# Performance work log

Hardware: AMD Instinct MI355X
Metric: run time of the kernel (lower is better)

Reference implementation:

```python
import jax, jax.numpy as jnp
import numpy as np

D_IN = 768
D_OUT = 768
NUM_HEADS = 12
HEAD_DIM = D_OUT // NUM_HEADS


def setup_inputs() -> dict:
    key = jax.random.key(0)
    ks = jax.random.split(key, 6)
    s = 1.0 / np.sqrt(D_IN)
    X = jax.random.normal(ks[0], (4, 2048, D_IN), dtype=jnp.float32)
    Wq = jax.random.uniform(ks[1], (D_IN, D_OUT), jnp.float32, -s, s)
    Wk = jax.random.uniform(ks[2], (D_IN, D_OUT), jnp.float32, -s, s)
    Wv = jax.random.uniform(ks[3], (D_IN, D_OUT), jnp.float32, -s, s)
    Wo = jax.random.uniform(ks[4], (D_OUT, D_OUT), jnp.float32, -s, s)
    bo = jax.random.uniform(ks[5], (D_OUT,), jnp.float32, -s, s)
    return {"X": X, "Wq": Wq, "Wk": Wk, "Wv": Wv, "Wo": Wo, "bo": bo}


def reference(X, Wq, Wk, Wv, Wo, bo):
    b, n, _ = X.shape
    # QKV projections, split heads -> [b, h, n, d]
    def split(t):
        return t.reshape(b, n, NUM_HEADS, HEAD_DIM).transpose(0, 2, 1, 3)
    q = split(X @ Wq)
    k = split(X @ Wk)
    v = split(X @ Wv)
    scores = jnp.einsum('bhqd,bhkd->bhqk', q, k) / np.sqrt(HEAD_DIM).astype(np.float32)
    causal = jnp.triu(jnp.ones((n, n), dtype=bool), k=1)
    scores = jnp.where(causal, -jnp.inf, scores)
    attn = jax.nn.softmax(scores, axis=-1)  # dropout p=0 -> identity
    ctx = jnp.einsum('bhqk,bhkd->bhqd', attn, v)
    ctx = ctx.transpose(0, 2, 1, 3).reshape(b, n, D_OUT)
    return ctx @ Wo + bo
```

## Files before the change

### kernel.cpp

```cpp
#include <hip/hip_runtime.h>
#include <stdint.h>

#define B_  4
#define N_  2048
#define D_  768
#define H_  12
#define HD_ 64
#define M_  (B_*N_)

typedef short bf8 __attribute__((ext_vector_type(8)));
typedef float f32x4 __attribute__((ext_vector_type(4)));

static __device__ __forceinline__ unsigned short f2bf(float f) {
    unsigned u = __float_as_uint(f);
    unsigned r = u + 0x7fffu + ((u >> 16) & 1u);
    return (unsigned short)(r >> 16);
}

static __device__ __forceinline__ unsigned pk2bf(float f0, float f1) {
    return ((__float_as_uint(f1) + 0x8000u) & 0xFFFF0000u) |
           ((__float_as_uint(f0) + 0x8000u) >> 16);
}

#if __has_builtin(__builtin_amdgcn_exp2f)
#define EXP2(x) __builtin_amdgcn_exp2f(x)
#else
#define EXP2(x) exp2f(x)
#endif

#define GLOAD_LDS16(gptr, lptr)                                                   \
    __builtin_amdgcn_global_load_lds(                                             \
        (const __attribute__((address_space(1))) void*)(gptr),                    \
        (__attribute__((address_space(3))) void*)(lptr), 16, 0, 0)

#define QSCALE 0.1803368801111204f

__global__ __launch_bounds__(256) void convert_x(const float* __restrict__ X,
                                                 unsigned short* __restrict__ Xb) {
    const size_t i = ((size_t)blockIdx.x * 256 + threadIdx.x) * 8;
    const float4 a = *(const float4*)(X + i);
    const float4 b = *(const float4*)(X + i + 4);
    ushort4 lo, hi;
    lo.x = f2bf(a.x); lo.y = f2bf(a.y); lo.z = f2bf(a.z); lo.w = f2bf(a.w);
    hi.x = f2bf(b.x); hi.y = f2bf(b.y); hi.z = f2bf(b.z); hi.w = f2bf(b.w);
    *(ushort4*)(Xb + i)     = lo;
    *(ushort4*)(Xb + i + 4) = hi;
}

__global__ __launch_bounds__(256) void transpose_w(
    const float* __restrict__ Wq, const float* __restrict__ Wk,
    const float* __restrict__ Wv, const float* __restrict__ Wo,
    unsigned short* __restrict__ Wqt, unsigned short* __restrict__ Wkt,
    unsigned short* __restrict__ Wvt, unsigned short* __restrict__ Wot)
{
    __shared__ float tile[32][33];
    const int z = blockIdx.z;
    const float* W = (z == 0) ? Wq : (z == 1) ? Wk : (z == 2) ? Wv : Wo;
    unsigned short* Wt = (z == 0) ? Wqt : (z == 1) ? Wkt : (z == 2) ? Wvt : Wot;
    const int k0 = blockIdx.x * 32, n0 = blockIdx.y * 32;
    const int tx = threadIdx.x & 31, ty = threadIdx.x >> 5;
    #pragma unroll
    for (int i = 0; i < 4; ++i)
        tile[ty + 8 * i][tx] = W[(size_t)(k0 + ty + 8 * i) * D_ + n0 + tx];
    __syncthreads();
    #pragma unroll
    for (int i = 0; i < 4; ++i)
        Wt[(size_t)(n0 + ty + 8 * i) * D_ + k0 + tx] = f2bf(tile[tx][ty + 8 * i]);
}

__global__ __launch_bounds__(256) void qkv_mfma(
    const unsigned short* __restrict__ Xb,
    const unsigned short* __restrict__ Wqt, const unsigned short* __restrict__ Wkt,
    const unsigned short* __restrict__ Wvt,
    unsigned short* __restrict__ Qb, unsigned short* __restrict__ Kb,
    unsigned short* __restrict__ Vt)
{
    __shared__ unsigned short As[128 * 32];
    __shared__ unsigned short Bs[128 * 32];

    const int t = threadIdx.x;
    const int wave = t >> 6, lane = t & 63;
    const int col = lane & 15, quad = lane >> 4;
    const int wm = (wave & 1) * 64, wn = (wave >> 1) * 64;

    const int m0 = blockIdx.x * 128;
    const int n0 = blockIdx.y * 128;
    const int mat = blockIdx.z;
    const unsigned short* Wt = (mat == 0) ? Wqt : (mat == 1) ? Wkt : Wvt;

    const unsigned short* Ag0 = Xb + (size_t)(m0 + (t >> 2)) * D_ + (t & 3) * 8;
    const unsigned short* Ag1 = Ag0 + (size_t)64 * D_;
    const unsigned short* Bg0 = Wt + (size_t)(n0 + (t >> 2)) * D_ + (t & 3) * 8;
    const unsigned short* Bg1 = Bg0 + (size_t)64 * D_;
    unsigned short* AsW0 = As + wave * 512;
    unsigned short* AsW1 = As + 2048 + wave * 512;
    unsigned short* BsW0 = Bs + wave * 512;
    unsigned short* BsW1 = Bs + 2048 + wave * 512;

    f32x4 acc[4][4] = {};

    for (int k0 = 0; k0 < D_; k0 += 32) {
        __syncthreads();
        GLOAD_LDS16(Ag0 + k0, AsW0);
        GLOAD_LDS16(Ag1 + k0, AsW1);
        GLOAD_LDS16(Bg0 + k0, BsW0);
        GLOAD_LDS16(Bg1 + k0, BsW1);
        __syncthreads();

        bf8 a[4], b[4];
        #pragma unroll
        for (int i = 0; i < 4; ++i)
            a[i] = *(const bf8*)(As + (wm + i * 16 + col) * 32 + quad * 8);
        #pragma unroll
        for (int j = 0; j < 4; ++j)
            b[j] = *(const bf8*)(Bs + (wn + j * 16 + col) * 32 + quad * 8);
        #pragma unroll
        for (int i = 0; i < 4; ++i)
            #pragma unroll
            for (int j = 0; j < 4; ++j)
                acc[i][j] = __builtin_amdgcn_mfma_f32_16x16x32_bf16(a[i], b[j], acc[i][j], 0, 0, 0);
    }

    if (mat != 2) {
        unsigned short* Out = (mat == 0) ? Qb : Kb;
        const float qsc = (mat == 0) ? QSCALE : 1.0f;
        #pragma unroll
        for (int j = 0; j < 4; ++j) {
            const int n = n0 + wn + j * 16 + col;
            const int h = n >> 6, d = n & 63;
            #pragma unroll
            for (int i = 0; i < 4; ++i) {
                const int mb = m0 + wm + i * 16 + quad * 4;
                const int bb = mb >> 11, nn = mb & (N_ - 1);
                unsigned short* op = Out + ((size_t)(bb * H_ + h) * N_ + nn) * HD_ + d;
                #pragma unroll
                for (int r = 0; r < 4; ++r) op[(size_t)r * HD_] = f2bf(acc[i][j][r] * qsc);
            }
        }
    } else {
        #pragma unroll
        for (int j = 0; j < 4; ++j) {
            const int n = n0 + wn + j * 16 + col;
            const int h = n >> 6, d = n & 63;
            #pragma unroll
            for (int i = 0; i < 4; ++i) {
                const int mb = m0 + wm + i * 16 + quad * 4;
                const int bb = mb >> 11, nn = mb & (N_ - 1);
                ushort4 pk;
                pk.x = f2bf(acc[i][j][0]); pk.y = f2bf(acc[i][j][1]);
                pk.z = f2bf(acc[i][j][2]); pk.w = f2bf(acc[i][j][3]);
                *(ushort4*)(Vt + ((size_t)(bb * H_ + h) * HD_ + d) * N_ + nn) = pk;
            }
        }
    }
}

#define PS 72

static __device__ __forceinline__ void qk_softmax(
    const bf8 (&ka)[4][2], bf8 qb0, bf8 qb1,
    int k0, int q, bool mask, float& lpart,
    unsigned short* Pw, int col, int quad)
{
    f32x4 s[4] = {};
    #pragma unroll
    for (int kc = 0; kc < 4; ++kc) {
        s[kc] = __builtin_amdgcn_mfma_f32_16x16x32_bf16(ka[kc][0], qb0, s[kc], 0, 0, 0);
        s[kc] = __builtin_amdgcn_mfma_f32_16x16x32_bf16(ka[kc][1], qb1, s[kc], 0, 0, 0);
    }

    float p[4][4];
    if (mask) {
        #pragma unroll
        for (int kc = 0; kc < 4; ++kc)
            #pragma unroll
            for (int r = 0; r < 4; ++r) {
                const int key = k0 + kc * 16 + quad * 4 + r;
                p[kc][r] = EXP2((key > q) ? -INFINITY : s[kc][r]);
            }
    } else {
        #pragma unroll
        for (int kc = 0; kc < 4; ++kc)
            #pragma unroll
            for (int r = 0; r < 4; ++r) p[kc][r] = EXP2(s[kc][r]);
    }

    #pragma unroll
    for (int kc = 0; kc < 4; ++kc)
        #pragma unroll
        for (int r = 0; r < 4; ++r) lpart += p[kc][r];

    #pragma unroll
    for (int kc = 0; kc < 4; ++kc) {
        uint2 pk;
        pk.x = pk2bf(p[kc][0], p[kc][1]);
        pk.y = pk2bf(p[kc][2], p[kc][3]);
        *(uint2*)(Pw + col * PS + kc * 16 + quad * 4) = pk;
    }
}

static __device__ __forceinline__ void pv_acc(
    const unsigned short* Pw, const bf8 (&va)[4][2],
    f32x4 (&o)[4], int col, int quad)
{
    const bf8 pb0 = *(const bf8*)(Pw + col * PS + quad * 8);
    const bf8 pb1 = *(const bf8*)(Pw + col * PS + 32 + quad * 8);
    #pragma unroll
    for (int dc = 0; dc < 4; ++dc) {
        o[dc] = __builtin_amdgcn_mfma_f32_16x16x32_bf16(va[dc][0], pb0, o[dc], 0, 0, 0);
        o[dc] = __builtin_amdgcn_mfma_f32_16x16x32_bf16(va[dc][1], pb1, o[dc], 0, 0, 0);
    }
}

__global__ __launch_bounds__(256, 3) void attn_mfma(
    const unsigned short* __restrict__ Qb,
    const unsigned short* __restrict__ Kb,
    const unsigned short* __restrict__ Vt,
    unsigned short* __restrict__ Ctxb)
{
    __shared__ unsigned short Kl[64 * PS];
    __shared__ unsigned short Vl[64 * PS];
    __shared__ unsigned short Pl[4][16 * PS];

    const int t = threadIdx.x;
    const int wave = t >> 6;
    const int lane = t & 63;
    const int col  = lane & 15;
    const int quad = lane >> 4;

    const int bid = blockIdx.x;
    const int bh  = bid >> 4;
    const int x   = bid & 15;
    const int tl  = x, th = 31 - x;
    const int q0L = tl * 64 + wave * 16;
    const int q0H = th * 64 + wave * 16;
    const int qL  = q0L + col;
    const int qH  = q0H + col;

    const unsigned short* Kp = Kb + (size_t)bh * N_ * HD_;
    const unsigned short* Vp = Vt + (size_t)bh * HD_ * N_;
    const unsigned short* QpL = Qb + ((size_t)bh * N_ + q0L) * HD_;
    const unsigned short* QpH = Qb + ((size_t)bh * N_ + q0H) * HD_;

    const bf8 qbL0 = *(const bf8*)(QpL + (size_t)col * HD_ + quad * 8);
    const bf8 qbL1 = *(const bf8*)(QpL + (size_t)col * HD_ + 32 + quad * 8);
    const bf8 qbH0 = *(const bf8*)(QpH + (size_t)col * HD_ + quad * 8);
    const bf8 qbH1 = *(const bf8*)(QpH + (size_t)col * HD_ + 32 + quad * 8);

    f32x4 oL[4] = {}, oH[4] = {};
    float lL = 0.f, lH = 0.f;

    unsigned short* Pw = &Pl[wave][0];

    const int srow = t >> 3;
    const int scol = (t & 7) * 8;
    const unsigned short* Kg = Kp + (size_t)srow * HD_ + scol;
    const unsigned short* Vg = Vp + (size_t)srow * N_ + scol;
    unsigned short* KlD0 = Kl + srow * PS + scol;
    unsigned short* KlD1 = Kl + (srow + 32) * PS + scol;
    unsigned short* VlD0 = Vl + srow * PS + scol;
    unsigned short* VlD1 = Vl + (srow + 32) * PS + scol;

    uint4 kr0 = *(const uint4*)(Kg);
    uint4 kr1 = *(const uint4*)(Kg + (size_t)32 * HD_);
    uint4 vr0 = *(const uint4*)(Vg);
    uint4 vr1 = *(const uint4*)(Vg + (size_t)32 * N_);

    const int iters = 32 - x;
    for (int kt = 0; kt < iters; ++kt) {
        const int k0 = kt * 64;
        const bool actL = (kt <= tl);

        *(uint4*)KlD0 = kr0;
        *(uint4*)KlD1 = kr1;
        *(uint4*)VlD0 = vr0;
        *(uint4*)VlD1 = vr1;
        __syncthreads();

        if (kt + 1 < iters) {
            const size_t k1 = (size_t)(k0 + 64);
            kr0 = *(const uint4*)(Kg + k1 * HD_);
            kr1 = *(const uint4*)(Kg + (k1 + 32) * HD_);
            vr0 = *(const uint4*)(Vg + k1);
            vr1 = *(const uint4*)(Vg + (size_t)32 * N_ + k1);
        }

        bf8 ka[4][2];
        #pragma unroll
        for (int kc = 0; kc < 4; ++kc) {
            ka[kc][0] = *(const bf8*)(Kl + (kc * 16 + col) * PS + quad * 8);
            ka[kc][1] = *(const bf8*)(Kl + (kc * 16 + col) * PS + 32 + quad * 8);
        }

        qk_softmax(ka, qbH0, qbH1, k0, qH, kt == th, lH, Pw, col, quad);

        bf8 va[4][2];
        #pragma unroll
        for (int dc = 0; dc < 4; ++dc) {
            va[dc][0] = *(const bf8*)(Vl + (dc * 16 + col) * PS + quad * 8);
            va[dc][1] = *(const bf8*)(Vl + (dc * 16 + col) * PS + 32 + quad * 8);
        }

        pv_acc(Pw, va, oH, col, quad);

        if (actL) {
            qk_softmax(ka, qbL0, qbL1, k0, qL, kt == tl, lL, Pw, col, quad);
            pv_acc(Pw, va, oL, col, quad);
        }

        __syncthreads();
    }

    const int b = bh / H_;
    const int h = bh % H_;
    {
        float l = lH;
        l += __shfl_xor(l, 16, 64);
        l += __shfl_xor(l, 32, 64);
        const float inv = 1.0f / l;
        unsigned short* cp = Ctxb + ((size_t)(b * N_ + qH)) * D_ + h * HD_;
        #pragma unroll
        for (int dc = 0; dc < 4; ++dc) {
            uint2 pk;
            pk.x = pk2bf(oH[dc][0] * inv, oH[dc][1] * inv);
            pk.y = pk2bf(oH[dc][2] * inv, oH[dc][3] * inv);
            *(uint2*)(cp + dc * 16 + quad * 4) = pk;
        }
    }
    {
        float l = lL;
        l += __shfl_xor(l, 16, 64);
        l += __shfl_xor(l, 32, 64);
        const float inv = 1.0f / l;
        unsigned short* cp = Ctxb + ((size_t)(b * N_ + qL)) * D_ + h * HD_;
        #pragma unroll
        for (int dc = 0; dc < 4; ++dc) {
            uint2 pk;
            pk.x = pk2bf(oL[dc][0] * inv, oL[dc][1] * inv);
            pk.y = pk2bf(oL[dc][2] * inv, oL[dc][3] * inv);
            *(uint2*)(cp + dc * 16 + quad * 4) = pk;
        }
    }
}

__global__ __launch_bounds__(256) void out_mfma(
    const unsigned short* __restrict__ Ctxb,
    const unsigned short* __restrict__ Wot,
    const float* __restrict__ bo,
    float* __restrict__ Out)
{
    __shared__ unsigned short As[128 * 32];
    __shared__ unsigned short Bs[128 * 32];

    const int t = threadIdx.x;
    const int wave = t >> 6, lane = t & 63;
    const int col = lane & 15, quad = lane >> 4;
    const int wm = (wave & 1) * 64, wn = (wave >> 1) * 64;

    const int m0 = blockIdx.x * 128;
    const int n0 = blockIdx.y * 128;

    const unsigned short* Ag0 = Ctxb + (size_t)(m0 + (t >> 2)) * D_ + (t & 3) * 8;
    const unsigned short* Ag1 = Ag0 + (size_t)64 * D_;
    const unsigned short* Bg0 = Wot + (size_t)(n0 + (t >> 2)) * D_ + (t & 3) * 8;
    const unsigned short* Bg1 = Bg0 + (size_t)64 * D_;
    unsigned short* AsW0 = As + wave * 512;
    unsigned short* AsW1 = As + 2048 + wave * 512;
    unsigned short* BsW0 = Bs + wave * 512;
    unsigned short* BsW1 = Bs + 2048 + wave * 512;

    f32x4 acc[4][4] = {};

    for (int k0 = 0; k0 < D_; k0 += 32) {
        __syncthreads();
        GLOAD_LDS16(Ag0 + k0, AsW0);
        GLOAD_LDS16(Ag1 + k0, AsW1);
        GLOAD_LDS16(Bg0 + k0, BsW0);
        GLOAD_LDS16(Bg1 + k0, BsW1);
        __syncthreads();

        bf8 a[4], b[4];
        #pragma unroll
        for (int i = 0; i < 4; ++i)
            a[i] = *(const bf8*)(As + (wm + i * 16 + col) * 32 + quad * 8);
        #pragma unroll
        for (int j = 0; j < 4; ++j)
            b[j] = *(const bf8*)(Bs + (wn + j * 16 + col) * 32 + quad * 8);
        #pragma unroll
        for (int i = 0; i < 4; ++i)
            #pragma unroll
            for (int j = 0; j < 4; ++j)
                acc[i][j] = __builtin_amdgcn_mfma_f32_16x16x32_bf16(a[i], b[j], acc[i][j], 0, 0, 0);
    }

    #pragma unroll
    for (int j = 0; j < 4; ++j) {
        const int n = n0 + wn + j * 16 + col;
        const float bias = bo[n];
        #pragma unroll
        for (int i = 0; i < 4; ++i) {
            const int mb = m0 + wm + i * 16 + quad * 4;
            #pragma unroll
            for (int r = 0; r < 4; ++r)
                Out[(size_t)(mb + r) * D_ + n] = acc[i][j][r] + bias;
        }
    }
}

extern "C" void kernel_launch(void* const* d_in, const int* in_sizes, int n_in,
                              void* d_out, int out_size, void* d_ws, size_t ws_size,
                              hipStream_t stream) {
    const float* X  = (const float*)d_in[0];
    const float* Wq = (const float*)d_in[1];
    const float* Wk = (const float*)d_in[2];
    const float* Wv = (const float*)d_in[3];
    const float* Wo = (const float*)d_in[4];
    const float* bo = (const float*)d_in[5];
    float* out = (float*)d_out;

    const size_t elems = (size_t)M_ * D_;
    const size_t welems = (size_t)D_ * D_;
    unsigned short* Xb  = (unsigned short*)d_ws;
    unsigned short* Wqt = Xb + elems;
    unsigned short* Wkt = Wqt + welems;
    unsigned short* Wvt = Wkt + welems;
    unsigned short* Wot = Wvt + welems;
    unsigned short* Qb  = Wot + welems;
    unsigned short* Kb  = Qb + elems;
    unsigned short* Vt  = Kb + elems;
    unsigned short* Ctxb = Xb;

    convert_x<<<dim3(elems / 2048), 256, 0, stream>>>(X, Xb);
    transpose_w<<<dim3(24, 24, 4), 256, 0, stream>>>(Wq, Wk, Wv, Wo, Wqt, Wkt, Wvt, Wot);

    qkv_mfma<<<dim3(M_ / 128, D_ / 128, 3), 256, 0, stream>>>(Xb, Wqt, Wkt, Wvt, Qb, Kb, Vt);

    attn_mfma<<<dim3(B_ * H_ * 16), 256, 0, stream>>>(Qb, Kb, Vt, Ctxb);

    out_mfma<<<dim3(M_ / 128, D_ / 128), 256, 0, stream>>>(Ctxb, Wot, bo, out);
}
```

Baseline: 214.5 us.

## Fuse X bf16 conversion into QKV GEMM with register-prefetched padded LDS tiles

Removes the separate convert_x kernel: the QKV GEMM now reads fp32 X directly, converts it to bf16 in registers and stores it into padded LDS tiles. Both GEMMs replace direct global-to-LDS loads with a register prefetch of the next K tile that overlaps the MFMA work, and pad the LDS row stride to reduce bank conflicts. Occupancy hints are added. The trade-off is that X is re-read in fp32 by each of the 18 column-block/matrix tiles, doubling its read bytes, in exchange for saving one kernel launch and the Xb write and read. The rounding also changes from round-to-nearest-even to a simpler round-half-up.

```diff
diff --git a/kernel.cpp b/kernel.cpp
--- a/kernel.cpp
+++ b/kernel.cpp
@@ -28,24 +28,9 @@
 #define EXP2(x) exp2f(x)
 #endif
 
-#define GLOAD_LDS16(gptr, lptr)                                                   \
-    __builtin_amdgcn_global_load_lds(                                             \
-        (const __attribute__((address_space(1))) void*)(gptr),                    \
-        (__attribute__((address_space(3))) void*)(lptr), 16, 0, 0)
-
 #define QSCALE 0.1803368801111204f
 
-__global__ __launch_bounds__(256) void convert_x(const float* __restrict__ X,
-                                                 unsigned short* __restrict__ Xb) {
-    const size_t i = ((size_t)blockIdx.x * 256 + threadIdx.x) * 8;
-    const float4 a = *(const float4*)(X + i);
-    const float4 b = *(const float4*)(X + i + 4);
-    ushort4 lo, hi;
-    lo.x = f2bf(a.x); lo.y = f2bf(a.y); lo.z = f2bf(a.z); lo.w = f2bf(a.w);
-    hi.x = f2bf(b.x); hi.y = f2bf(b.y); hi.z = f2bf(b.z); hi.w = f2bf(b.w);
-    *(ushort4*)(Xb + i)     = lo;
-    *(ushort4*)(Xb + i + 4) = hi;
-}
+#define TS 40
 
 __global__ __launch_bounds__(256) void transpose_w(
     const float* __restrict__ Wq, const float* __restrict__ Wk,
@@ -68,15 +53,15 @@
         Wt[(size_t)(n0 + ty + 8 * i) * D_ + k0 + tx] = f2bf(tile[tx][ty + 8 * i]);
 }
 
-__global__ __launch_bounds__(256) void qkv_mfma(
-    const unsigned short* __restrict__ Xb,
+__global__ __launch_bounds__(256, 3) void qkv_mfma(
+    const float* __restrict__ X,
     const unsigned short* __restrict__ Wqt, const unsigned short* __restrict__ Wkt,
     const unsigned short* __restrict__ Wvt,
     unsigned short* __restrict__ Qb, unsigned short* __restrict__ Kb,
     unsigned short* __restrict__ Vt)
 {
-    __shared__ unsigned short As[128 * 32];
-    __shared__ unsigned short Bs[128 * 32];
+    __shared__ unsigned short As[128 * TS];
+    __shared__ unsigned short Bs[128 * TS];
 
     const int t = threadIdx.x;
     const int wave = t >> 6, lane = t & 63;
@@ -88,37 +73,56 @@
     const int mat = blockIdx.z;
     const unsigned short* Wt = (mat == 0) ? Wqt : (mat == 1) ? Wkt : Wvt;
 
-    const unsigned short* Ag0 = Xb + (size_t)(m0 + (t >> 2)) * D_ + (t & 3) * 8;
-    const unsigned short* Ag1 = Ag0 + (size_t)64 * D_;
-    const unsigned short* Bg0 = Wt + (size_t)(n0 + (t >> 2)) * D_ + (t & 3) * 8;
-    const unsigned short* Bg1 = Bg0 + (size_t)64 * D_;
-    unsigned short* AsW0 = As + wave * 512;
-    unsigned short* AsW1 = As + 2048 + wave * 512;
-    unsigned short* BsW0 = Bs + wave * 512;
-    unsigned short* BsW1 = Bs + 2048 + wave * 512;
+    const int srow = t >> 1;
+    const int shalf = (t & 1) * 16;
+    const float* Ag = X + (size_t)(m0 + srow) * D_ + shalf;
+    const unsigned short* Bg = Wt + (size_t)(n0 + srow) * D_ + shalf;
+    unsigned short* AsD = As + srow * TS + shalf;
+    unsigned short* BsD = Bs + srow * TS + shalf;
+
+    float4 af0 = *(const float4*)(Ag);
+    float4 af1 = *(const float4*)(Ag + 4);
+    float4 af2 = *(const float4*)(Ag + 8);
+    float4 af3 = *(const float4*)(Ag + 12);
+    uint4  bf0 = *(const uint4*)(Bg);
+    uint4  bf1 = *(const uint4*)(Bg + 8);
 
     f32x4 acc[4][4] = {};
 
     for (int k0 = 0; k0 < D_; k0 += 32) {
-        __syncthreads();
-        GLOAD_LDS16(Ag0 + k0, AsW0);
-        GLOAD_LDS16(Ag1 + k0, AsW1);
-        GLOAD_LDS16(Bg0 + k0, BsW0);
-        GLOAD_LDS16(Bg1 + k0, BsW1);
-        __syncthreads();
+        uint4 ap0, ap1;
+        ap0.x = pk2bf(af0.x, af0.y); ap0.y = pk2bf(af0.z, af0.w);
+        ap0.z = pk2bf(af1.x, af1.y); ap0.w = pk2bf(af1.z, af1.w);
+        ap1.x = pk2bf(af2.x, af2.y); ap1.y = pk2bf(af2.z, af2.w);
+        ap1.z = pk2bf(af3.x, af3.y); ap1.w = pk2bf(af3.z, af3.w);
+        *(uint4*)(AsD)     = ap0;
+        *(uint4*)(AsD + 8) = ap1;
+        *(uint4*)(BsD)     = bf0;
+        *(uint4*)(BsD + 8) = bf1;
+        __syncthreads();
+
+        if (k0 + 32 < D_) {
+            af0 = *(const float4*)(Ag + k0 + 32);
+            af1 = *(const float4*)(Ag + k0 + 36);
+            af2 = *(const float4*)(Ag + k0 + 40);
+            af3 = *(const float4*)(Ag + k0 + 44);
+            bf0 = *(const uint4*)(Bg + k0 + 32);
+            bf1 = *(const uint4*)(Bg + k0 + 40);
+        }
 
         bf8 a[4], b[4];
         #pragma unroll
         for (int i = 0; i < 4; ++i)
-            a[i] = *(const bf8*)(As + (wm + i * 16 + col) * 32 + quad * 8);
+            a[i] = *(const bf8*)(As + (wm + i * 16 + col) * TS + quad * 8);
         #pragma unroll
         for (int j = 0; j < 4; ++j)
-            b[j] = *(const bf8*)(Bs + (wn + j * 16 + col) * 32 + quad * 8);
+            b[j] = *(const bf8*)(Bs + (wn + j * 16 + col) * TS + quad * 8);
         #pragma unroll
         for (int i = 0; i < 4; ++i)
             #pragma unroll
             for (int j = 0; j < 4; ++j)
                 acc[i][j] = __builtin_amdgcn_mfma_f32_16x16x32_bf16(a[i], b[j], acc[i][j], 0, 0, 0);
+        __syncthreads();
     }
 
     if (mat != 2) {
@@ -343,14 +347,14 @@
     }
 }
 
-__global__ __launch_bounds__(256) void out_mfma(
+__global__ __launch_bounds__(256, 3) void out_mfma(
     const unsigned short* __restrict__ Ctxb,
     const unsigned short* __restrict__ Wot,
     const float* __restrict__ bo,
     float* __restrict__ Out)
 {
-    __shared__ unsigned short As[128 * 32];
-    __shared__ unsigned short Bs[128 * 32];
+    __shared__ unsigned short As[128 * TS];
+    __shared__ unsigned short Bs[128 * TS];
 
     const int t = threadIdx.x;
     const int wave = t >> 6, lane = t & 63;
@@ -360,37 +364,47 @@
     const int m0 = blockIdx.x * 128;
     const int n0 = blockIdx.y * 128;
 
-    const unsigned short* Ag0 = Ctxb + (size_t)(m0 + (t >> 2)) * D_ + (t & 3) * 8;
-    const unsigned short* Ag1 = Ag0 + (size_t)64 * D_;
-    const unsigned short* Bg0 = Wot + (size_t)(n0 + (t >> 2)) * D_ + (t & 3) * 8;
-    const unsigned short* Bg1 = Bg0 + (size_t)64 * D_;
-    unsigned short* AsW0 = As + wave * 512;
-    unsigned short* AsW1 = As + 2048 + wave * 512;
-    unsigned short* BsW0 = Bs + wave * 512;
-    unsigned short* BsW1 = Bs + 2048 + wave * 512;
+    const int srow = t >> 1;
+    const int shalf = (t & 1) * 16;
+    const unsigned short* Ag = Ctxb + (size_t)(m0 + srow) * D_ + shalf;
+    const unsigned short* Bg = Wot + (size_t)(n0 + srow) * D_ + shalf;
+    unsigned short* AsD = As + srow * TS + shalf;
+    unsigned short* BsD = Bs + srow * TS + shalf;
+
+    uint4 ar0 = *(const uint4*)(Ag);
+    uint4 ar1 = *(const uint4*)(Ag + 8);
+    uint4 br0 = *(const uint4*)(Bg);
+    uint4 br1 = *(const uint4*)(Bg + 8);
 
     f32x4 acc[4][4] = {};
 
     for (int k0 = 0; k0 < D_; k0 += 32) {
-        __syncthreads();
-        GLOAD_LDS16(Ag0 + k0, AsW0);
-        GLOAD_LDS16(Ag1 + k0, AsW1);
-        GLOAD_LDS16(Bg0 + k0, BsW0);
-        GLOAD_LDS16(Bg1 + k0, BsW1);
-        __syncthreads();
+        *(uint4*)(AsD)     = ar0;
+        *(uint4*)(AsD + 8) = ar1;
+        *(uint4*)(BsD)     = br0;
+        *(uint4*)(BsD + 8) = br1;
+        __syncthreads();
+
+        if (k0 + 32 < D_) {
+            ar0 = *(const uint4*)(Ag + k0 + 32);
+            ar1 = *(const uint4*)(Ag + k0 + 40);
+            br0 = *(const uint4*)(Bg + k0 + 32);
+            br1 = *(const uint4*)(Bg + k0 + 40);
+        }
 
         bf8 a[4], b[4];
         #pragma unroll
         for (int i = 0; i < 4; ++i)
-            a[i] = *(const bf8*)(As + (wm + i * 16 + col) * 32 + quad * 8);
+            a[i] = *(const bf8*)(As + (wm + i * 16 + col) * TS + quad * 8);
         #pragma unroll
         for (int j = 0; j < 4; ++j)
-            b[j] = *(const bf8*)(Bs + (wn + j * 16 + col) * 32 + quad * 8);
+            b[j] = *(const bf8*)(Bs + (wn + j * 16 + col) * TS + quad * 8);
         #pragma unroll
         for (int i = 0; i < 4; ++i)
             #pragma unroll
             for (int j = 0; j < 4; ++j)
                 acc[i][j] = __builtin_amdgcn_mfma_f32_16x16x32_bf16(a[i], b[j], acc[i][j], 0, 0, 0);
+        __syncthreads();
     }
 
     #pragma unroll
@@ -420,20 +434,18 @@
 
     const size_t elems = (size_t)M_ * D_;
     const size_t welems = (size_t)D_ * D_;
-    unsigned short* Xb  = (unsigned short*)d_ws;
-    unsigned short* Wqt = Xb + elems;
+    unsigned short* Wqt = (unsigned short*)d_ws;
     unsigned short* Wkt = Wqt + welems;
     unsigned short* Wvt = Wkt + welems;
     unsigned short* Wot = Wvt + welems;
     unsigned short* Qb  = Wot + welems;
     unsigned short* Kb  = Qb + elems;
     unsigned short* Vt  = Kb + elems;
-    unsigned short* Ctxb = Xb;
-
-    convert_x<<<dim3(elems / 2048), 256, 0, stream>>>(X, Xb);
+    unsigned short* Ctxb = Vt + elems;
+
     transpose_w<<<dim3(24, 24, 4), 256, 0, stream>>>(Wq, Wk, Wv, Wo, Wqt, Wkt, Wvt, Wot);
 
-    qkv_mfma<<<dim3(M_ / 128, D_ / 128, 3), 256, 0, stream>>>(Xb, Wqt, Wkt, Wvt, Qb, Kb, Vt);
+    qkv_mfma<<<dim3(M_ / 128, D_ / 128, 3), 256, 0, stream>>>(X, Wqt, Wkt, Wvt, Qb, Kb, Vt);
 
     attn_mfma<<<dim3(B_ * H_ * 16), 256, 0, stream>>>(Qb, Kb, Vt, Ctxb);
 
```

Result: no change. 216.6 us (+1.0%).
